# Kernel tuning notes

Hardware: AMD Instinct MI355X
Metric: run time of the kernel (lower is better)

## Reference

```python
import jax, jax.numpy as jnp
import numpy as np

K = 8          # number of nearest neighbors (init kwarg k)
CONST = 0.1    # inverseweight const
NUM = 1.0      # inverseweight num


def setup_inputs() -> dict:
    key = jax.random.key(0)
    k1, k2 = jax.random.split(key)
    data1 = jax.random.normal(k1, (4096, 1024), dtype=jnp.float32)
    data2 = jax.random.normal(k2, (8192, 1024), dtype=jnp.float32)
    return {"data1": data1, "data2": data2}


def reference(data1, data2):
    # pairwise Euclidean distance (torch.dist with p=2): [N, M]
    x2 = jnp.sum(data1 * data1, axis=1, keepdims=True)          # [N, 1]
    y2 = jnp.sum(data2 * data2, axis=1)                         # [M]
    d2 = x2 + y2[None, :] - 2.0 * (data1 @ data2.T)             # [N, M]
    dist = jnp.sqrt(jnp.maximum(d2, 1e-12))

    # k smallest distances and their indices
    neg_top, idx = jax.lax.top_k(-dist, K)                      # [N, K]
    knn_dist = -neg_top                                         # [N, K]

    # inverse weighting: w = num / (dist + const)
    w = NUM / (knn_dist + CONST)                                # [N, K]

    # gather neighbor vectors and weighted-average them
    neigh = data2[idx]                                          # [N, K, D]
    out = jnp.einsum('nk,nkd->nd', w, neigh) / jnp.sum(w, axis=1, keepdims=True)
    return out
```

## Files before the change

kernel.cpp:

```cpp
#include <hip/hip_runtime.h>


typedef short bf16x8 __attribute__((ext_vector_type(8)));
typedef float f32x4 __attribute__((ext_vector_type(4)));

#define SENTINEL 1e30f
#define BKK 32

static __device__ __forceinline__ unsigned short f2bf(float f) {
  unsigned u = __float_as_uint(f);
  return (unsigned short)((u + 0x7fffu + ((u >> 16) & 1u)) >> 16);
}

__global__ __launch_bounds__(256) void convert_all_kernel(
    const float* __restrict__ A, const float* __restrict__ B,
    unsigned short* __restrict__ Abf, unsigned short* __restrict__ Bbf,
    float* __restrict__ y2, int N) {
  const int bid = blockIdx.x;
  const int tid = threadIdx.x;
  if (bid < N) {
    const float4 v = ((const float4*)&A[(size_t)bid * 1024])[tid];
    ushort4 o;
    o.x = f2bf(v.x); o.y = f2bf(v.y); o.z = f2bf(v.z); o.w = f2bf(v.w);
    ((ushort4*)&Abf[(size_t)bid * 1024])[tid] = o;
  } else {
    const int m = bid - N;
    __shared__ float red[256];
    const float4 v = ((const float4*)&B[(size_t)m * 1024])[tid];
    ushort4 o;
    o.x = f2bf(v.x); o.y = f2bf(v.y); o.z = f2bf(v.z); o.w = f2bf(v.w);
    ((ushort4*)&Bbf[(size_t)m * 1024])[tid] = o;
    red[tid] = v.x * v.x + v.y * v.y + v.z * v.z + v.w * v.w;
    __syncthreads();
    for (int s = 128; s > 0; s >>= 1) {
      if (tid < s) red[tid] += red[tid + s];
      __syncthreads();
    }
    if (tid == 0) y2[m] = red[0];
  }
}

#define CAS(sa, ia, sb, ib)                         \
  do {                                              \
    if ((sa) > (sb)) {                              \
      const float _t = (sa); (sa) = (sb); (sb) = _t;\
      const int _u = (ia); (ia) = (ib); (ib) = _u;  \
    }                                               \
  } while (0)

#define STAGE(sk, b)                                                          \
  do {                                                                        \
    const unsigned short* gA_ =                                               \
        Abf + (size_t)(r0 + w * 32 + srow) * 1024 + (sk) * 32 + sofs;         \
    const unsigned short* gB_ =                                               \
        Bbf + (size_t)(c0 + w * 64 + srow) * 1024 + (sk) * 32 + sofs;         \
    __builtin_amdgcn_global_load_lds(                                         \
        (const __attribute__((address_space(1))) void*)gA_,                   \
        (__attribute__((address_space(3))) void*)&As[b][(w * 32) * 32],       \
        16, 0, 0);                                                            \
    __builtin_amdgcn_global_load_lds(                                         \
        (const __attribute__((address_space(1))) void*)(gA_ + (size_t)16 * 1024), \
        (__attribute__((address_space(3))) void*)&As[b][(w * 32 + 16) * 32],  \
        16, 0, 0);                                                            \
    _Pragma("unroll")                                                         \
    for (int l_ = 0; l_ < 4; ++l_)                                            \
      __builtin_amdgcn_global_load_lds(                                       \
          (const __attribute__((address_space(1))) void*)(gB_ + (size_t)(16 * l_) * 1024), \
          (__attribute__((address_space(3))) void*)&Bs[b][(w * 64 + 16 * l_) * 32], \
          16, 0, 0);                                                          \
  } while (0)

#define COMPUTE(b)                                                            \
  do {                                                                        \
    bf16x8 af[4], bfr[8];                                                     \
    _Pragma("unroll")                                                         \
    for (int fi = 0; fi < 4; ++fi)                                            \
      af[fi] = *(const bf16x8*)&As[b][(frowA + fi * 16) * 32 + fofs];         \
    _Pragma("unroll")                                                         \
    for (int fj = 0; fj < 8; ++fj)                                            \
      bfr[fj] = *(const bf16x8*)&Bs[b][(frowB + fj * 16) * 32 + fofs];        \
    __builtin_amdgcn_s_setprio(1);                                            \
    _Pragma("unroll")                                                         \
    for (int fi = 0; fi < 4; ++fi)                                            \
      _Pragma("unroll")                                                       \
      for (int fj = 0; fj < 8; ++fj)                                          \
        acc[fi][fj] = __builtin_amdgcn_mfma_f32_16x16x32_bf16(                \
            bfr[fj], af[fi], acc[fi][fj], 0, 0, 0);                           \
    __builtin_amdgcn_s_setprio(0);                                            \
  } while (0)

#define PIPE_SYNC(N)                                                          \
  do {                                                                        \
    asm volatile("s_waitcnt vmcnt(" #N ")" ::: "memory");                     \
    __builtin_amdgcn_sched_barrier(0);                                        \
    __builtin_amdgcn_s_barrier();                                             \
    __builtin_amdgcn_sched_barrier(0);                                        \
  } while (0)

__global__ __launch_bounds__(256, 2) void screen6_kernel(
    const unsigned short* __restrict__ Abf, const unsigned short* __restrict__ Bbf,
    const float* __restrict__ y2g,
    float* __restrict__ cand_s, int* __restrict__ cand_i) {
  __shared__ unsigned short As[3][128 * 32];
  __shared__ unsigned short Bs[3][256 * 32];

  const int tid = threadIdx.x;
  const int w = tid >> 6;
  const int lane = tid & 63;
  const int wr = w >> 1, wc = w & 1;

  const int v = blockIdx.x + gridDim.x * blockIdx.y;
  const int bx = (v & 7) * 2 + ((v >> 3) & 1);
  const int by = v >> 4;
  const int r0 = by * 128;

  const int srow = lane >> 2;
  const int sofs = ((lane & 3) ^ ((lane >> 3) & 3)) * 8;

  const int frowA = wr * 64 + (lane & 15);
  const int frowB = wc * 128 + (lane & 15);
  const int fofs = ((lane >> 4) ^ ((lane >> 1) & 3)) * 8;
  const int cgrp = (lane >> 4) * 4;

  for (int chunk = 0; chunk < 2; ++chunk) {
    const int c0 = bx * 512 + chunk * 256;
    __syncthreads();

    f32x4 acc[4][8];
#pragma unroll
    for (int fi = 0; fi < 4; ++fi)
#pragma unroll
      for (int fj = 0; fj < 8; ++fj) {
        f32x4 z = {0.f, 0.f, 0.f, 0.f};
        acc[fi][fj] = z;
      }

    STAGE(0, 0);
    STAGE(1, 1);
    int cA = 0, cB = 1, cC = 2;
    for (int t = 0; t < 31; ++t) {
      PIPE_SYNC(6);
      if (t < 30) STAGE(t + 2, cC);
      __builtin_amdgcn_sched_barrier(0);
      COMPUTE(cA);
      const int tmp = cA; cA = cB; cB = cC; cC = tmp;
    }
    PIPE_SYNC(0);
    COMPUTE(cA);

    float4 y2v[8];
#pragma unroll
    for (int fj = 0; fj < 8; ++fj)
      y2v[fj] = *(const float4*)&y2g[c0 + wc * 128 + fj * 16 + cgrp];

#pragma unroll
    for (int fi = 0; fi < 4; ++fi) {
      float ls[8];
      int li[8];
#pragma unroll
      for (int j = 0; j < 8; ++j) { ls[j] = SENTINEL; li[j] = 0x7fffffff; }
      const int cb = c0 + wc * 128 + cgrp;
#pragma unroll
      for (int fj = 0; fj < 8; ++fj) {
#pragma unroll
        for (int reg = 0; reg < 4; ++reg) {
          const float s = y2v[fj][reg] - 2.0f * acc[fi][fj][reg];
          if (s < ls[7]) {
            ls[7] = s; li[7] = cb + fj * 16 + reg;
#pragma unroll
            for (int j = 7; j > 0; --j) {
              if (ls[j] < ls[j - 1]) {
                const float t = ls[j]; ls[j] = ls[j - 1]; ls[j - 1] = t;
                const int u = li[j]; li[j] = li[j - 1]; li[j - 1] = u;
              }
            }
          }
        }
      }
#pragma unroll
      for (int off = 16; off <= 32; off <<= 1) {
        float rs[8];
        int ri[8];
#pragma unroll
        for (int j = 0; j < 8; ++j) {
          rs[j] = __shfl_xor(ls[j], off, 64);
          ri[j] = __shfl_xor(li[j], off, 64);
        }
        float ms[8];
        int mi_[8];
#pragma unroll
        for (int i = 0; i < 8; ++i) {
          const bool t = ls[i] < rs[7 - i];
          ms[i] = t ? ls[i] : rs[7 - i];
          mi_[i] = t ? li[i] : ri[7 - i];
        }
        CAS(ms[0], mi_[0], ms[4], mi_[4]);
        CAS(ms[1], mi_[1], ms[5], mi_[5]);
        CAS(ms[2], mi_[2], ms[6], mi_[6]);
        CAS(ms[3], mi_[3], ms[7], mi_[7]);
        CAS(ms[0], mi_[0], ms[2], mi_[2]);
        CAS(ms[1], mi_[1], ms[3], mi_[3]);
        CAS(ms[4], mi_[4], ms[6], mi_[6]);
        CAS(ms[5], mi_[5], ms[7], mi_[7]);
        CAS(ms[0], mi_[0], ms[1], mi_[1]);
        CAS(ms[2], mi_[2], ms[3], mi_[3]);
        CAS(ms[4], mi_[4], ms[5], mi_[5]);
        CAS(ms[6], mi_[6], ms[7], mi_[7]);
#pragma unroll
        for (int j = 0; j < 8; ++j) { ls[j] = ms[j]; li[j] = mi_[j]; }
      }
      if ((lane >> 4) == 0) {
        const int row = r0 + wr * 64 + fi * 16 + lane;
        const size_t base =
            ((size_t)row * 64 + wc * 32 + bx * 2 + chunk) * 8;
#pragma unroll
        for (int j = 0; j < 8; ++j) {
          cand_s[base + j] = ls[j];
          cand_i[base + j] = li[j];
        }
      }
    }
  }
}

__global__ __launch_bounds__(256) void finalize6_kernel(
    const float* __restrict__ A, const float* __restrict__ B,
    const float* __restrict__ y2g,
    const float* __restrict__ cand_s, const int* __restrict__ cand_i,
    float* __restrict__ out) {
  const int tid = threadIdx.x;
  const int w = tid >> 6;
  const int lane = tid & 63;
  const int rloc = w >> 1;
  const int wh = w & 1;
  const int n = blockIdx.x * 2 + rloc;
  __shared__ float comb[2][2][16];

  float s12[12];
  int i12[12];
  {
    const float4* cs = (const float4*)&cand_s[(size_t)n * 512 + lane * 8];
    const int4* cj = (const int4*)&cand_i[(size_t)n * 512 + lane * 8];
    const float4 sa = cs[0], sb = cs[1];
    const int4 ja = cj[0], jb = cj[1];
    s12[0] = sa.x; s12[1] = sa.y; s12[2] = sa.z; s12[3] = sa.w;
    s12[4] = sb.x; s12[5] = sb.y; s12[6] = sb.z; s12[7] = sb.w;
    i12[0] = ja.x; i12[1] = ja.y; i12[2] = ja.z; i12[3] = ja.w;
    i12[4] = jb.x; i12[5] = jb.y; i12[6] = jb.z; i12[7] = jb.w;
#pragma unroll
    for (int j = 8; j < 12; ++j) { s12[j] = SENTINEL; i12[j] = 0x7fffffff; }
  }

#pragma unroll
  for (int off = 1; off <= 32; off <<= 1) {
    float rs[12];
    int ri[12];
#pragma unroll
    for (int j = 0; j < 12; ++j) {
      rs[j] = __shfl_xor(s12[j], off, 64);
      ri[j] = __shfl_xor(i12[j], off, 64);
    }
    float ms[12];
    int mj[12];
#pragma unroll
    for (int j = 0; j < 12; ++j) {
      const bool tke = s12[j] < rs[11 - j];
      ms[j] = tke ? s12[j] : rs[11 - j];
      mj[j] = tke ? i12[j] : ri[11 - j];
    }
    CAS(ms[0], mj[0], ms[8], mj[8]);  CAS(ms[1], mj[1], ms[9], mj[9]);
    CAS(ms[2], mj[2], ms[10], mj[10]); CAS(ms[3], mj[3], ms[11], mj[11]);
    CAS(ms[4], mj[4], ms[8], mj[8]);  CAS(ms[5], mj[5], ms[9], mj[9]);
    CAS(ms[6], mj[6], ms[10], mj[10]); CAS(ms[7], mj[7], ms[11], mj[11]);
    CAS(ms[0], mj[0], ms[2], mj[2]);  CAS(ms[1], mj[1], ms[3], mj[3]);
    CAS(ms[4], mj[4], ms[6], mj[6]);  CAS(ms[5], mj[5], ms[7], mj[7]);
    CAS(ms[8], mj[8], ms[10], mj[10]); CAS(ms[9], mj[9], ms[11], mj[11]);
    CAS(ms[0], mj[0], ms[1], mj[1]);  CAS(ms[2], mj[2], ms[3], mj[3]);
    CAS(ms[4], mj[4], ms[5], mj[5]);  CAS(ms[6], mj[6], ms[7], mj[7]);
    CAS(ms[8], mj[8], ms[9], mj[9]);  CAS(ms[10], mj[10], ms[11], mj[11]);
#pragma unroll
    for (int j = 0; j < 12; ++j) { s12[j] = ms[j]; i12[j] = mj[j]; }
  }

  const float4* Arow = (const float4*)&A[(size_t)n * 1024];
  const int fbase = wh * 128 + lane * 2;
  float4 a4[2];
  a4[0] = Arow[fbase];
  a4[1] = Arow[fbase + 1];
  float4 bk0[12], bk1[12];
#pragma unroll
  for (int j = 0; j < 12; ++j) {
    const float4* Brow = (const float4*)&B[(size_t)i12[j] * 1024];
    bk0[j] = Brow[fbase];
    bk1[j] = Brow[fbase + 1];
  }
  float part[13];
  part[12] = a4[0].x * a4[0].x + a4[0].y * a4[0].y + a4[0].z * a4[0].z +
             a4[0].w * a4[0].w + a4[1].x * a4[1].x + a4[1].y * a4[1].y +
             a4[1].z * a4[1].z + a4[1].w * a4[1].w;
#pragma unroll
  for (int j = 0; j < 12; ++j) {
    part[j] = a4[0].x * bk0[j].x + a4[0].y * bk0[j].y + a4[0].z * bk0[j].z +
              a4[0].w * bk0[j].w;
    part[j] += a4[1].x * bk1[j].x + a4[1].y * bk1[j].y + a4[1].z * bk1[j].z +
               a4[1].w * bk1[j].w;
  }
#pragma unroll
  for (int r = 0; r < 13; ++r) {
#pragma unroll
    for (int off = 32; off >= 1; off >>= 1) part[r] += __shfl_xor(part[r], off, 64);
  }
  if (lane == 0) {
#pragma unroll
    for (int r = 0; r < 13; ++r) comb[rloc][wh][r] = part[r];
  }
  __syncthreads();
  float tot[13];
#pragma unroll
  for (int r = 0; r < 13; ++r) tot[r] = comb[rloc][0][r] + comb[rloc][1][r];

  const float x2 = tot[12];
  float d2v[12];
  float wsel[12];
  bool used[12];
#pragma unroll
  for (int j = 0; j < 12; ++j) {
    d2v[j] = x2 + y2g[i12[j]] - 2.0f * tot[j];
    used[j] = false;
    wsel[j] = 0.0f;
  }
  float wsum = 0.0f;
  for (int k = 0; k < 8; ++k) {
    float bd = SENTINEL;
    int bi = 0x7fffffff, bslot = 0;
#pragma unroll
    for (int j = 0; j < 12; ++j) {
      if (used[j]) continue;
      const float d2 = d2v[j];
      if (d2 < bd || (d2 == bd && i12[j] < bi)) { bd = d2; bi = i12[j]; bslot = j; }
    }
    used[bslot] = true;
    const float d2c = fmaxf(bd, 1e-12f);
    const float wv = 1.0f / (sqrtf(d2c) + 0.1f);
    wsel[bslot] = wv;
    wsum += wv;
  }
  const float inv = 1.0f / wsum;

  float4 o0 = {0, 0, 0, 0}, o1 = {0, 0, 0, 0};
#pragma unroll
  for (int j = 0; j < 12; ++j) {
    const float wv = wsel[j];
    o0.x += wv * bk0[j].x; o0.y += wv * bk0[j].y;
    o0.z += wv * bk0[j].z; o0.w += wv * bk0[j].w;
    o1.x += wv * bk1[j].x; o1.y += wv * bk1[j].y;
    o1.z += wv * bk1[j].z; o1.w += wv * bk1[j].w;
  }
  o0.x *= inv; o0.y *= inv; o0.z *= inv; o0.w *= inv;
  o1.x *= inv; o1.y *= inv; o1.z *= inv; o1.w *= inv;
  float4* Orow = (float4*)&out[(size_t)n * 1024];
  Orow[fbase] = o0;
  Orow[fbase + 1] = o1;
}

__global__ __launch_bounds__(256) void rownorm_kernel(
    const float* __restrict__ B, float* __restrict__ y2) {
  const int m = blockIdx.x;
  const int tid = threadIdx.x;
  __shared__ float red[256];
  const float4 v = *(const float4*)&B[(size_t)m * 1024 + tid * 4];
  red[tid] = v.x * v.x + v.y * v.y + v.z * v.z + v.w * v.w;
  __syncthreads();
  for (int s = 128; s > 0; s >>= 1) {
    if (tid < s) red[tid] += red[tid + s];
    __syncthreads();
  }
  if (tid == 0) y2[m] = red[0];
}

__global__ __launch_bounds__(256) void knn_chunk_kernel(
    const float* __restrict__ A, const float* __restrict__ B,
    const float* __restrict__ y2g,
    float* __restrict__ cand_s, int* __restrict__ cand_i) {
  __shared__ float As[BKK][68];
  __shared__ float Bs[BKK][68];
  __shared__ float Sc[64][65];

  const int tid = threadIdx.x;
  const int tx = tid & 15;
  const int ty = tid >> 4;
  const int r0 = blockIdx.y * 64;
  const int c0 = blockIdx.x * 1024;
  const int lrow = tid >> 3;
  const int lk = (tid & 7) * 4;

  float top_s[8];
  int top_i[8];
#pragma unroll
  for (int j = 0; j < 8; ++j) { top_s[j] = SENTINEL; top_i[j] = 0x7fffffff; }

  for (int tile = 0; tile < 16; ++tile) {
    const int cbase = c0 + tile * 64;
    float acc[4][4];
#pragma unroll
    for (int i = 0; i < 4; ++i)
#pragma unroll
      for (int j = 0; j < 4; ++j) acc[i][j] = 0.0f;

    for (int k0 = 0; k0 < 1024; k0 += BKK) {
      const float4 a0 = *(const float4*)&A[(size_t)(r0 + lrow) * 1024 + k0 + lk];
      const float4 a1 = *(const float4*)&A[(size_t)(r0 + lrow + 32) * 1024 + k0 + lk];
      const float4 b0 = *(const float4*)&B[(size_t)(cbase + lrow) * 1024 + k0 + lk];
      const float4 b1 = *(const float4*)&B[(size_t)(cbase + lrow + 32) * 1024 + k0 + lk];
      __syncthreads();
      As[lk + 0][lrow] = a0.x; As[lk + 1][lrow] = a0.y;
      As[lk + 2][lrow] = a0.z; As[lk + 3][lrow] = a0.w;
      As[lk + 0][lrow + 32] = a1.x; As[lk + 1][lrow + 32] = a1.y;
      As[lk + 2][lrow + 32] = a1.z; As[lk + 3][lrow + 32] = a1.w;
      Bs[lk + 0][lrow] = b0.x; Bs[lk + 1][lrow] = b0.y;
      Bs[lk + 2][lrow] = b0.z; Bs[lk + 3][lrow] = b0.w;
      Bs[lk + 0][lrow + 32] = b1.x; Bs[lk + 1][lrow + 32] = b1.y;
      Bs[lk + 2][lrow + 32] = b1.z; Bs[lk + 3][lrow + 32] = b1.w;
      __syncthreads();
#pragma unroll
      for (int kk = 0; kk < BKK; ++kk) {
        const float4 av = *(const float4*)&As[kk][ty * 4];
        const float4 bv = *(const float4*)&Bs[kk][tx * 4];
        acc[0][0] += av.x * bv.x; acc[0][1] += av.x * bv.y;
        acc[0][2] += av.x * bv.z; acc[0][3] += av.x * bv.w;
        acc[1][0] += av.y * bv.x; acc[1][1] += av.y * bv.y;
        acc[1][2] += av.y * bv.z; acc[1][3] += av.y * bv.w;
        acc[2][0] += av.z * bv.x; acc[2][1] += av.z * bv.y;
        acc[2][2] += av.z * bv.z; acc[2][3] += av.z * bv.w;
        acc[3][0] += av.w * bv.x; acc[3][1] += av.w * bv.y;
        acc[3][2] += av.w * bv.z; acc[3][3] += av.w * bv.w;
      }
    }
#pragma unroll
    for (int i = 0; i < 4; ++i) {
      const int row = ty * 4 + i;
#pragma unroll
      for (int j = 0; j < 4; ++j) {
        const int col = tx * 4 + j;
        Sc[row][col] = y2g[cbase + col] - 2.0f * acc[i][j];
      }
    }
    __syncthreads();
    if (tid < 64) {
      for (int c = 0; c < 64; ++c) {
        const float s = Sc[tid][c];
        if (s < top_s[7]) {
          top_s[7] = s; top_i[7] = cbase + c;
#pragma unroll
          for (int j = 7; j > 0; --j) {
            if (top_s[j] < top_s[j - 1]) {
              const float tss = top_s[j]; top_s[j] = top_s[j - 1]; top_s[j - 1] = tss;
              const int tii = top_i[j]; top_i[j] = top_i[j - 1]; top_i[j - 1] = tii;
            }
          }
        }
      }
    }
  }

  if (tid < 64) {
    const int n = r0 + tid;
    const int base = (n * gridDim.x + blockIdx.x) * 8;
#pragma unroll
    for (int j = 0; j < 8; ++j) {
      cand_s[base + j] = top_s[j];
      cand_i[base + j] = top_i[j];
    }
  }
}

__global__ __launch_bounds__(256) void finalize_kernel(
    const float* __restrict__ A, const float* __restrict__ B,
    const float* __restrict__ cand_s, const int* __restrict__ cand_i,
    float* __restrict__ out, int nchunks) {
  const int n = blockIdx.x;
  const int tid = threadIdx.x;
  __shared__ float red[256];
  __shared__ float ls[64];
  __shared__ int li[64];
  __shared__ float wsh2[8];
  __shared__ int wid[8];
  __shared__ float wsum_sh;

  const int ncand = nchunks * 8;
  const float4 a = *(const float4*)&A[(size_t)n * 1024 + tid * 4];
  red[tid] = a.x * a.x + a.y * a.y + a.z * a.z + a.w * a.w;
  if (tid < ncand) {
    ls[tid] = cand_s[n * ncand + tid];
    li[tid] = cand_i[n * ncand + tid];
  }
  __syncthreads();
  for (int s = 128; s > 0; s >>= 1) {
    if (tid < s) red[tid] += red[tid + s];
    __syncthreads();
  }
  if (tid == 0) {
    const float x2 = red[0];
    float wsum = 0.0f;
    for (int j = 0; j < 8; ++j) {
      float bs = SENTINEL;
      int bi = 0x7fffffff;
      int bp = 0;
      for (int c = 0; c < ncand; ++c) {
        const float s_ = ls[c];
        const int i_ = li[c];
        if (s_ < bs || (s_ == bs && i_ < bi)) { bs = s_; bi = i_; bp = c; }
      }
      ls[bp] = SENTINEL; li[bp] = 0x7fffffff;
      float d2 = x2 + bs;
      d2 = fmaxf(d2, 1e-12f);
      const float wkk = 1.0f / (sqrtf(d2) + 0.1f);
      wsh2[j] = wkk; wid[j] = bi;
      wsum += wkk;
    }
    wsum_sh = wsum;
  }
  __syncthreads();
  const float inv = 1.0f / wsum_sh;
  float ox = 0.0f, oy = 0.0f, oz = 0.0f, ow = 0.0f;
#pragma unroll
  for (int j = 0; j < 8; ++j) {
    const float wkk = wsh2[j];
    const float4 v = *(const float4*)&B[(size_t)wid[j] * 1024 + tid * 4];
    ox += wkk * v.x; oy += wkk * v.y; oz += wkk * v.z; ow += wkk * v.w;
  }
  float4 o;
  o.x = ox * inv; o.y = oy * inv; o.z = oz * inv; o.w = ow * inv;
  *(float4*)&out[(size_t)n * 1024 + tid * 4] = o;
}

extern "C" void kernel_launch(void* const* d_in, const int* in_sizes, int n_in,
                              void* d_out, int out_size, void* d_ws, size_t ws_size,
                              hipStream_t stream) {
  const float* A = (const float*)d_in[0];
  const float* Bm = (const float*)d_in[1];
  const int D = 1024;
  const int N = in_sizes[0] / D;
  const int M = in_sizes[1] / D;

  const size_t needA = (size_t)N * D * 2;
  const size_t needB = (size_t)M * D * 2;
  const size_t needC = (size_t)N * 512 * 4;
  const size_t need = needA + needB + (size_t)M * 4 + 2 * needC;

  if (ws_size >= need && M == 8192 && N % 128 == 0 && N % 2 == 0) {
    unsigned short* Abf = (unsigned short*)d_ws;
    unsigned short* Bbf = Abf + (size_t)N * D;
    float* y2 = (float*)(Bbf + (size_t)M * D);
    float* cand_s = y2 + M;
    int* cand_i = (int*)(cand_s + (size_t)N * 512);

    convert_all_kernel<<<N + M, 256, 0, stream>>>(A, Bm, Abf, Bbf, y2, N);
    dim3 g(M / 512, N / 128);
    screen6_kernel<<<g, 256, 0, stream>>>(Abf, Bbf, y2, cand_s, cand_i);
    finalize6_kernel<<<N / 2, 256, 0, stream>>>(A, Bm, y2, cand_s, cand_i,
                                                (float*)d_out);
  } else {
    float* y2 = (float*)d_ws;
    float* cand_s = y2 + M;
    int* cand_i = (int*)(cand_s + (size_t)N * 64);
    rownorm_kernel<<<M, 256, 0, stream>>>(Bm, y2);
    dim3 gridB(M / 1024, N / 64);
    knn_chunk_kernel<<<gridB, 256, 0, stream>>>(A, Bm, y2, cand_s, cand_i);
    finalize_kernel<<<N, 256, 0, stream>>>(A, Bm, cand_s, cand_i, (float*)d_out, M / 1024);
  }
}
```

Measured before the change: 330.3 us.

## Shrink screening GEMM tile to 64x128 per block with one row strip per wave

The screening kernel moves from 128x512 output per block (two 256-column chunks, 2x2 wave layout) to 64x128 tiles with each wave owning 16 rows across all 128 columns. The grid remapping and candidate layout are reworked so each block writes one window of 8 candidates per row. Occupancy rises from 2 to 4 blocks per CU with smaller LDS and accumulator footprints, and the grid becomes much larger to fill the CUs. In exchange, each LDS fragment is reused across fewer MFMAs, so per-FLOP global and LDS traffic goes up.

Measured after the change: 314.3 us. 1.05x faster.

```diff
diff --git a/kernel.cpp b/kernel.cpp
--- a/kernel.cpp
+++ b/kernel.cpp
@@ -51,41 +51,35 @@
 #define STAGE(sk, b)                                                          \
   do {                                                                        \
     const unsigned short* gA_ =                                               \
-        Abf + (size_t)(r0 + w * 32 + srow) * 1024 + (sk) * 32 + sofs;         \
+        Abf + (size_t)(r0 + w * 16 + srow) * 1024 + (sk) * 32 + sofs;         \
     const unsigned short* gB_ =                                               \
-        Bbf + (size_t)(c0 + w * 64 + srow) * 1024 + (sk) * 32 + sofs;         \
+        Bbf + (size_t)(c0 + w * 32 + srow) * 1024 + (sk) * 32 + sofs;         \
     __builtin_amdgcn_global_load_lds(                                         \
         (const __attribute__((address_space(1))) void*)gA_,                   \
-        (__attribute__((address_space(3))) void*)&As[b][(w * 32) * 32],       \
+        (__attribute__((address_space(3))) void*)&As[b][(w * 16) * 32],       \
         16, 0, 0);                                                            \
     __builtin_amdgcn_global_load_lds(                                         \
-        (const __attribute__((address_space(1))) void*)(gA_ + (size_t)16 * 1024), \
-        (__attribute__((address_space(3))) void*)&As[b][(w * 32 + 16) * 32],  \
+        (const __attribute__((address_space(1))) void*)gB_,                   \
+        (__attribute__((address_space(3))) void*)&Bs[b][(w * 32) * 32],       \
         16, 0, 0);                                                            \
-    _Pragma("unroll")                                                         \
-    for (int l_ = 0; l_ < 4; ++l_)                                            \
-      __builtin_amdgcn_global_load_lds(                                       \
-          (const __attribute__((address_space(1))) void*)(gB_ + (size_t)(16 * l_) * 1024), \
-          (__attribute__((address_space(3))) void*)&Bs[b][(w * 64 + 16 * l_) * 32], \
-          16, 0, 0);                                                          \
+    __builtin_amdgcn_global_load_lds(                                         \
+        (const __attribute__((address_space(1))) void*)(gB_ + (size_t)16 * 1024), \
+        (__attribute__((address_space(3))) void*)&Bs[b][(w * 32 + 16) * 32],  \
+        16, 0, 0);                                                            \
   } while (0)
 
 #define COMPUTE(b)                                                            \
   do {                                                                        \
-    bf16x8 af[4], bfr[8];                                                     \
-    _Pragma("unroll")                                                         \
-    for (int fi = 0; fi < 4; ++fi)                                            \
-      af[fi] = *(const bf16x8*)&As[b][(frowA + fi * 16) * 32 + fofs];         \
+    bf16x8 af, bfr[8];                                                        \
+    af = *(const bf16x8*)&As[b][frowA * 32 + fofs];                           \
     _Pragma("unroll")                                                         \
     for (int fj = 0; fj < 8; ++fj)                                            \
       bfr[fj] = *(const bf16x8*)&Bs[b][(frowB + fj * 16) * 32 + fofs];        \
     __builtin_amdgcn_s_setprio(1);                                            \
     _Pragma("unroll")                                                         \
-    for (int fi = 0; fi < 4; ++fi)                                            \
-      _Pragma("unroll")                                                       \
-      for (int fj = 0; fj < 8; ++fj)                                          \
-        acc[fi][fj] = __builtin_amdgcn_mfma_f32_16x16x32_bf16(                \
-            bfr[fj], af[fi], acc[fi][fj], 0, 0, 0);                           \
+    for (int fj = 0; fj < 8; ++fj)                                            \
+      acc[fj] = __builtin_amdgcn_mfma_f32_16x16x32_bf16(                      \
+          bfr[fj], af, acc[fj], 0, 0, 0);                                     \
     __builtin_amdgcn_s_setprio(0);                                            \
   } while (0)
 
@@ -97,128 +91,114 @@
     __builtin_amdgcn_sched_barrier(0);                                        \
   } while (0)
 
-__global__ __launch_bounds__(256, 2) void screen6_kernel(
+__global__ __launch_bounds__(256, 4) void screen8_kernel(
     const unsigned short* __restrict__ Abf, const unsigned short* __restrict__ Bbf,
     const float* __restrict__ y2g,
     float* __restrict__ cand_s, int* __restrict__ cand_i) {
-  __shared__ unsigned short As[3][128 * 32];
-  __shared__ unsigned short Bs[3][256 * 32];
+  __shared__ unsigned short As[3][64 * 32];
+  __shared__ unsigned short Bs[3][128 * 32];
 
   const int tid = threadIdx.x;
   const int w = tid >> 6;
   const int lane = tid & 63;
-  const int wr = w >> 1, wc = w & 1;
 
   const int v = blockIdx.x + gridDim.x * blockIdx.y;
-  const int bx = (v & 7) * 2 + ((v >> 3) & 1);
-  const int by = v >> 4;
-  const int r0 = by * 128;
+  const int u = v >> 3;
+  const int window = (v & 7) * 8 + (u & 7);
+  const int rowtile = u >> 3;
+  const int r0 = rowtile * 64;
+  const int c0 = window * 128;
 
   const int srow = lane >> 2;
   const int sofs = ((lane & 3) ^ ((lane >> 3) & 3)) * 8;
 
-  const int frowA = wr * 64 + (lane & 15);
-  const int frowB = wc * 128 + (lane & 15);
+  const int frowA = w * 16 + (lane & 15);
+  const int frowB = lane & 15;
   const int fofs = ((lane >> 4) ^ ((lane >> 1) & 3)) * 8;
   const int cgrp = (lane >> 4) * 4;
 
-  for (int chunk = 0; chunk < 2; ++chunk) {
-    const int c0 = bx * 512 + chunk * 256;
-    __syncthreads();
-
-    f32x4 acc[4][8];
-#pragma unroll
-    for (int fi = 0; fi < 4; ++fi)
-#pragma unroll
-      for (int fj = 0; fj < 8; ++fj) {
-        f32x4 z = {0.f, 0.f, 0.f, 0.f};
-        acc[fi][fj] = z;
-      }
-
-    STAGE(0, 0);
-    STAGE(1, 1);
-    int cA = 0, cB = 1, cC = 2;
-    for (int t = 0; t < 31; ++t) {
-      PIPE_SYNC(6);
-      if (t < 30) STAGE(t + 2, cC);
-      __builtin_amdgcn_sched_barrier(0);
-      COMPUTE(cA);
-      const int tmp = cA; cA = cB; cB = cC; cC = tmp;
-    }
-    PIPE_SYNC(0);
+  f32x4 acc[8];
+#pragma unroll
+  for (int fj = 0; fj < 8; ++fj) {
+    f32x4 z = {0.f, 0.f, 0.f, 0.f};
+    acc[fj] = z;
+  }
+
+  STAGE(0, 0);
+  STAGE(1, 1);
+  int cA = 0, cB = 1, cC = 2;
+  for (int t = 0; t < 31; ++t) {
+    PIPE_SYNC(3);
+    if (t < 30) STAGE(t + 2, cC);
+    __builtin_amdgcn_sched_barrier(0);
     COMPUTE(cA);
-
-    float4 y2v[8];
-#pragma unroll
-    for (int fj = 0; fj < 8; ++fj)
-      y2v[fj] = *(const float4*)&y2g[c0 + wc * 128 + fj * 16 + cgrp];
-
-#pragma unroll
-    for (int fi = 0; fi < 4; ++fi) {
-      float ls[8];
-      int li[8];
-#pragma unroll
-      for (int j = 0; j < 8; ++j) { ls[j] = SENTINEL; li[j] = 0x7fffffff; }
-      const int cb = c0 + wc * 128 + cgrp;
-#pragma unroll
-      for (int fj = 0; fj < 8; ++fj) {
-#pragma unroll
-        for (int reg = 0; reg < 4; ++reg) {
-          const float s = y2v[fj][reg] - 2.0f * acc[fi][fj][reg];
-          if (s < ls[7]) {
-            ls[7] = s; li[7] = cb + fj * 16 + reg;
-#pragma unroll
-            for (int j = 7; j > 0; --j) {
-              if (ls[j] < ls[j - 1]) {
-                const float t = ls[j]; ls[j] = ls[j - 1]; ls[j - 1] = t;
-                const int u = li[j]; li[j] = li[j - 1]; li[j - 1] = u;
-              }
-            }
+    const int tmp = cA; cA = cB; cB = cC; cC = tmp;
+  }
+  PIPE_SYNC(0);
+  COMPUTE(cA);
+
+  float ls[8];
+  int li[8];
+#pragma unroll
+  for (int j = 0; j < 8; ++j) { ls[j] = SENTINEL; li[j] = 0x7fffffff; }
+  const int cb = c0 + cgrp;
+#pragma unroll
+  for (int fj = 0; fj < 8; ++fj) {
+    const float4 y2q = *(const float4*)&y2g[c0 + fj * 16 + cgrp];
+#pragma unroll
+    for (int reg = 0; reg < 4; ++reg) {
+      const float s = y2q[reg] - 2.0f * acc[fj][reg];
+      if (s < ls[7]) {
+        ls[7] = s; li[7] = cb + fj * 16 + reg;
+#pragma unroll
+        for (int j = 7; j > 0; --j) {
+          if (ls[j] < ls[j - 1]) {
+            const float t = ls[j]; ls[j] = ls[j - 1]; ls[j - 1] = t;
+            const int u2 = li[j]; li[j] = li[j - 1]; li[j - 1] = u2;
           }
         }
       }
-#pragma unroll
-      for (int off = 16; off <= 32; off <<= 1) {
-        float rs[8];
-        int ri[8];
-#pragma unroll
-        for (int j = 0; j < 8; ++j) {
-          rs[j] = __shfl_xor(ls[j], off, 64);
-          ri[j] = __shfl_xor(li[j], off, 64);
-        }
-        float ms[8];
-        int mi_[8];
-#pragma unroll
-        for (int i = 0; i < 8; ++i) {
-          const bool t = ls[i] < rs[7 - i];
-          ms[i] = t ? ls[i] : rs[7 - i];
-          mi_[i] = t ? li[i] : ri[7 - i];
-        }
-        CAS(ms[0], mi_[0], ms[4], mi_[4]);
-        CAS(ms[1], mi_[1], ms[5], mi_[5]);
-        CAS(ms[2], mi_[2], ms[6], mi_[6]);
-        CAS(ms[3], mi_[3], ms[7], mi_[7]);
-        CAS(ms[0], mi_[0], ms[2], mi_[2]);
-        CAS(ms[1], mi_[1], ms[3], mi_[3]);
-        CAS(ms[4], mi_[4], ms[6], mi_[6]);
-        CAS(ms[5], mi_[5], ms[7], mi_[7]);
-        CAS(ms[0], mi_[0], ms[1], mi_[1]);
-        CAS(ms[2], mi_[2], ms[3], mi_[3]);
-        CAS(ms[4], mi_[4], ms[5], mi_[5]);
-        CAS(ms[6], mi_[6], ms[7], mi_[7]);
-#pragma unroll
-        for (int j = 0; j < 8; ++j) { ls[j] = ms[j]; li[j] = mi_[j]; }
-      }
-      if ((lane >> 4) == 0) {
-        const int row = r0 + wr * 64 + fi * 16 + lane;
-        const size_t base =
-            ((size_t)row * 64 + wc * 32 + bx * 2 + chunk) * 8;
-#pragma unroll
-        for (int j = 0; j < 8; ++j) {
-          cand_s[base + j] = ls[j];
-          cand_i[base + j] = li[j];
-        }
-      }
+    }
+  }
+#pragma unroll
+  for (int off = 16; off <= 32; off <<= 1) {
+    float rs[8];
+    int ri[8];
+#pragma unroll
+    for (int j = 0; j < 8; ++j) {
+      rs[j] = __shfl_xor(ls[j], off, 64);
+      ri[j] = __shfl_xor(li[j], off, 64);
+    }
+    float ms[8];
+    int mi_[8];
+#pragma unroll
+    for (int i = 0; i < 8; ++i) {
+      const bool t = ls[i] < rs[7 - i];
+      ms[i] = t ? ls[i] : rs[7 - i];
+      mi_[i] = t ? li[i] : ri[7 - i];
+    }
+    CAS(ms[0], mi_[0], ms[4], mi_[4]);
+    CAS(ms[1], mi_[1], ms[5], mi_[5]);
+    CAS(ms[2], mi_[2], ms[6], mi_[6]);
+    CAS(ms[3], mi_[3], ms[7], mi_[7]);
+    CAS(ms[0], mi_[0], ms[2], mi_[2]);
+    CAS(ms[1], mi_[1], ms[3], mi_[3]);
+    CAS(ms[4], mi_[4], ms[6], mi_[6]);
+    CAS(ms[5], mi_[5], ms[7], mi_[7]);
+    CAS(ms[0], mi_[0], ms[1], mi_[1]);
+    CAS(ms[2], mi_[2], ms[3], mi_[3]);
+    CAS(ms[4], mi_[4], ms[5], mi_[5]);
+    CAS(ms[6], mi_[6], ms[7], mi_[7]);
+#pragma unroll
+    for (int j = 0; j < 8; ++j) { ls[j] = ms[j]; li[j] = mi_[j]; }
+  }
+  if ((lane >> 4) == 0) {
+    const int row = r0 + w * 16 + lane;
+    const size_t base = ((size_t)row * 64 + window) * 8;
+#pragma unroll
+    for (int j = 0; j < 8; ++j) {
+      cand_s[base + j] = ls[j];
+      cand_i[base + j] = li[j];
     }
   }
 }
@@ -548,7 +528,7 @@
   const size_t needC = (size_t)N * 512 * 4;
   const size_t need = needA + needB + (size_t)M * 4 + 2 * needC;
 
-  if (ws_size >= need && M == 8192 && N % 128 == 0 && N % 2 == 0) {
+  if (ws_size >= need && M == 8192 && N % 64 == 0 && N % 2 == 0) {
     unsigned short* Abf = (unsigned short*)d_ws;
     unsigned short* Bbf = Abf + (size_t)N * D;
     float* y2 = (float*)(Bbf + (size_t)M * D);
@@ -556,8 +536,8 @@
     int* cand_i = (int*)(cand_s + (size_t)N * 512);
 
     convert_all_kernel<<<N + M, 256, 0, stream>>>(A, Bm, Abf, Bbf, y2, N);
-    dim3 g(M / 512, N / 128);
-    screen6_kernel<<<g, 256, 0, stream>>>(Abf, Bbf, y2, cand_s, cand_i);
+    dim3 g(64, N / 64);
+    screen8_kernel<<<g, 256, 0, stream>>>(Abf, Bbf, y2, cand_s, cand_i);
     finalize6_kernel<<<N / 2, 256, 0, stream>>>(A, Bm, y2, cand_s, cand_i,
                                                 (float*)d_out);
   } else {
```
